# Performance work log

Hardware: AMD Instinct MI355X
Metric: run time of the kernel (lower is better)

Reference implementation:

```python
import jax, jax.numpy as jnp
import numpy as np

B = 2048          # number of tables (real batch size)
C = 8             # columns per table
D = 768           # hidden size (BERT-base)
TEMP = 0.07       # hp.temp
NEG_FILL = -10.0


def setup_inputs() -> dict:
    key = jax.random.key(0)
    k1, k2, k3 = jax.random.split(key, 3)
    n = B * C
    z = jax.random.normal(k1, (2 * n, D), jnp.float32) * 0.05
    idx = jnp.repeat(jnp.arange(B, dtype=jnp.int32), C)  # contiguous segment ids, as torch.full per table
    query = jax.random.normal(k2, (D, 1), jnp.float32) * 0.05
    attn_temp = jnp.ones((), jnp.float32)
    W = jax.random.normal(k3, (D, D), jnp.float32) * 0.02
    b = jnp.zeros((D,), jnp.float32)
    return {"z": z, "ori_table_indices": idx, "aug_table_indices": idx,
            "query": query, "attn_temp": attn_temp, "W": W, "b": b}


def _attn_pool(z, idx, query, t):
    # scatter-softmax attention pooling over variable-size table segments
    scores = (z @ query)[:, 0] / t                               # [n]
    e = jnp.exp(scores - scores.max())
    denom = jax.ops.segment_sum(e, idx, num_segments=B)[idx]     # [n]
    w = e / (denom + 1e-8)
    return jax.ops.segment_sum(z * w[:, None], idx, num_segments=B)  # [B, D]


def reference(z, ori_table_indices, aug_table_indices, query, attn_temp, W, b):
    n = B * C
    z_ori, z_aug = z[:n], z[n:]
    gx = _attn_pool(z_ori, ori_table_indices, query, attn_temp) @ W.T + b  # [B, D]
    hx = _attn_pool(z_aug, aug_table_indices, query, attn_temp) @ W.T + b  # [B, D]
    f = jnp.concatenate([gx, hx], axis=0)                                  # [2B, D]
    f = f / jnp.linalg.norm(f, axis=1, keepdims=True)
    sim = f @ f.T                                                          # [2B, 2B]
    N = 2 * B
    lab = jnp.concatenate([jnp.arange(B), jnp.arange(B)])
    labels = lab[None, :] == lab[:, None]                                  # [N, N] bool
    potential_pos = (sim > 0.9) & (~labels)
    safe_neg = (~potential_pos) & (~labels)
    # remove diagonal via rotation gather (order of negatives is irrelevant: topk sorts)
    cols = (jnp.arange(N)[:, None] + jnp.arange(1, N)[None, :]) % N        # [N, N-1]
    sim_od = jnp.take_along_axis(sim, cols, axis=1)
    safe_od = jnp.take_along_axis(safe_neg, cols, axis=1)
    # each row's single positive is its paired view at column (i+B) mod N
    pos = jnp.take_along_axis(sim, ((jnp.arange(N) + B) % N)[:, None], axis=1)  # [N, 1]
    neg = jnp.where(safe_od, sim_od, NEG_FILL)
    # data-dependent k; static-shape topk via descending sort + column mask
    k = jnp.maximum(1, jnp.floor(0.5 * jnp.mean(jnp.sum(safe_od, axis=1).astype(jnp.float32))).astype(jnp.int32))
    sneg = -jnp.sort(-neg, axis=1)                                         # descending
    new_neg = jnp.where(jnp.arange(N - 1)[None, :] < k, sneg, NEG_FILL)
    logits = jnp.concatenate([pos, new_neg], axis=1) / TEMP                # [N, N]
    # cross-entropy with target class 0
    loss = jnp.mean(jax.nn.logsumexp(logits, axis=1) - logits[:, 0])
    return loss
```

## Files before the change

### kernel.cpp

```cpp
#include <hip/hip_runtime.h>
#include <hip/hip_bf16.h>
#include <math.h>

#define Bq   2048
#define Cq   8
#define Dq   768
#define NROW 16384
#define NTOT 32768
#define Nq   4096
#define TEMPq 0.07f

typedef __attribute__((ext_vector_type(8))) short bf16x8;
typedef __attribute__((ext_vector_type(4))) float f32x4;

__device__ __hip_bfloat16 g_pooledb[(size_t)Nq * Dq];
__device__ __hip_bfloat16 g_Wb[(size_t)Dq * Dq];
__device__ float          g_f[(size_t)Nq * Dq];
__device__ __hip_bfloat16 g_fb[(size_t)Nq * Dq];
__device__ float          g_sim[(size_t)Nq * Nq];
__device__ unsigned int   g_viol;
__device__ float          g_rowloss[Nq];

#define GLDS16(src, dst) __builtin_amdgcn_global_load_lds( \
    (const __attribute__((address_space(1))) void*)(src),  \
    (__attribute__((address_space(3))) void*)(dst), 16, 0, 0)

__global__ __launch_bounds__(256) void pool_fused_kernel(const float* __restrict__ z,
                                                         const float* __restrict__ query,
                                                         const float* __restrict__ attn_temp) {
    int seg  = (int)((blockIdx.x * blockDim.x + threadIdx.x) >> 6);
    int lane = threadIdx.x & 63;
    if (seg >= Nq) return;
    int half = seg >> 11;
    int b    = seg & 2047;
    int baseRow = half * NROW + b * Cq;
    float invt = 1.f / attn_temp[0];

    float4 q4[3];
#pragma unroll
    for (int j = 0; j < 3; ++j) q4[j] = *(const float4*)(query + j * 256 + lane * 4);

    float4 v4[Cq][3];
    float s[Cq];
#pragma unroll
    for (int c = 0; c < Cq; ++c) {
        const float* zr = z + (size_t)(baseRow + c) * Dq;
        float acc = 0.f;
#pragma unroll
        for (int j = 0; j < 3; ++j) {
            float4 vz = *(const float4*)(zr + j * 256 + lane * 4);
            v4[c][j] = vz;
            acc += vz.x * q4[j].x + vz.y * q4[j].y + vz.z * q4[j].z + vz.w * q4[j].w;
        }
#pragma unroll
        for (int o = 32; o > 0; o >>= 1) acc += __shfl_xor(acc, o, 64);
        s[c] = acc * invt;
    }
    float m = s[0];
#pragma unroll
    for (int c = 1; c < Cq; ++c) m = fmaxf(m, s[c]);
    float e[Cq], denom = 0.f;
#pragma unroll
    for (int c = 0; c < Cq; ++c) { e[c] = expf(s[c] - m); denom += e[c]; }
    float inv = 1.f / (denom + 1e-8f);
#pragma unroll
    for (int j = 0; j < 3; ++j) {
        float4 acc = {0.f, 0.f, 0.f, 0.f};
#pragma unroll
        for (int c = 0; c < Cq; ++c) {
            acc.x += v4[c][j].x * e[c];
            acc.y += v4[c][j].y * e[c];
            acc.z += v4[c][j].z * e[c];
            acc.w += v4[c][j].w * e[c];
        }
        short4 o;
        o.x = ((__hip_bfloat16_raw)__float2bfloat16(acc.x * inv)).x;
        o.y = ((__hip_bfloat16_raw)__float2bfloat16(acc.y * inv)).x;
        o.z = ((__hip_bfloat16_raw)__float2bfloat16(acc.z * inv)).x;
        o.w = ((__hip_bfloat16_raw)__float2bfloat16(acc.w * inv)).x;
        *(short4*)((short*)g_pooledb + (size_t)seg * Dq + j * 256 + lane * 4) = o;
    }
}

__global__ __launch_bounds__(256) void wconv_kernel(const float* __restrict__ W) {
    if (blockIdx.x == 0 && threadIdx.x == 0) g_viol = 0u;
    int i = blockIdx.x * 256 + threadIdx.x;
    float4 v = ((const float4*)W)[i];
    short4 o;
    o.x = ((__hip_bfloat16_raw)__float2bfloat16(v.x)).x;
    o.y = ((__hip_bfloat16_raw)__float2bfloat16(v.y)).x;
    o.z = ((__hip_bfloat16_raw)__float2bfloat16(v.z)).x;
    o.w = ((__hip_bfloat16_raw)__float2bfloat16(v.w)).x;
    ((short4*)g_Wb)[i] = o;
}

__global__ __launch_bounds__(256) void fw_mfma_kernel(const float* __restrict__ bias) {
    __shared__ short lA[128 * 32];
    __shared__ short lB[128 * 32];
    const int bm = blockIdx.y * 128;
    const int bn = blockIdx.x * 128;

    const int tid  = threadIdx.x;
    const int wave = tid >> 6, lane = tid & 63;
    const int wr = wave >> 1, wc = wave & 1;

    const short* A = (const short*)g_pooledb;
    const short* Bt = (const short*)g_Wb;

    const int c0 = wave * 2, c1 = wave * 2 + 1;
    const int srow = lane >> 2;
    const int scol = (lane & 3) * 8;

    f32x4 acc[4][4];
#pragma unroll
    for (int m = 0; m < 4; ++m)
#pragma unroll
        for (int n = 0; n < 4; ++n) acc[m][n] = (f32x4){0.f, 0.f, 0.f, 0.f};

    for (int k0 = 0; k0 < Dq; k0 += 32) {
        GLDS16(A  + (size_t)(bm + c0 * 16 + srow) * Dq + k0 + scol, lA + c0 * 512);
        GLDS16(A  + (size_t)(bm + c1 * 16 + srow) * Dq + k0 + scol, lA + c1 * 512);
        GLDS16(Bt + (size_t)(bn + c0 * 16 + srow) * Dq + k0 + scol, lB + c0 * 512);
        GLDS16(Bt + (size_t)(bn + c1 * 16 + srow) * Dq + k0 + scol, lB + c1 * 512);
        __syncthreads();

        bf16x8 af[4], bfr[4];
#pragma unroll
        for (int m = 0; m < 4; ++m) {
            int row = wr * 64 + m * 16 + (lane & 15);
            af[m] = *(const bf16x8*)(lA + row * 32 + (lane >> 4) * 8);
        }
#pragma unroll
        for (int n = 0; n < 4; ++n) {
            int row = wc * 64 + n * 16 + (lane & 15);
            bfr[n] = *(const bf16x8*)(lB + row * 32 + (lane >> 4) * 8);
        }
#pragma unroll
        for (int m = 0; m < 4; ++m)
#pragma unroll
            for (int n = 0; n < 4; ++n)
                acc[m][n] = __builtin_amdgcn_mfma_f32_16x16x32_bf16(af[m], bfr[n], acc[m][n], 0, 0, 0);
        __syncthreads();
    }

#pragma unroll
    for (int m = 0; m < 4; ++m) {
        int rowb = bm + wr * 64 + m * 16 + (lane >> 4) * 4;
#pragma unroll
        for (int n = 0; n < 4; ++n) {
            int col = bn + wc * 64 + n * 16 + (lane & 15);
            float bc = bias[col];
#pragma unroll
            for (int j = 0; j < 4; ++j)
                g_f[(size_t)(rowb + j) * Dq + col] = acc[m][n][j] + bc;
        }
    }
}

__global__ __launch_bounds__(256) void normalize_kernel() {
    int row  = (int)((blockIdx.x * blockDim.x + threadIdx.x) >> 6);
    int lane = threadIdx.x & 63;
    if (row >= Nq) return;
    float ss = 0.f;
    float v[Dq / 64];
#pragma unroll
    for (int j = 0; j < Dq / 64; ++j) { v[j] = g_f[(size_t)row * Dq + j * 64 + lane]; ss += v[j] * v[j]; }
#pragma unroll
    for (int o = 32; o > 0; o >>= 1) ss += __shfl_xor(ss, o, 64);
    float rn = 1.f / sqrtf(ss);
#pragma unroll
    for (int j = 0; j < Dq / 64; ++j)
        g_fb[(size_t)row * Dq + j * 64 + lane] = __float2bfloat16(v[j] * rn);
}

__global__ __launch_bounds__(256) void sim_mfma_kernel() {
    __shared__ short lA[128 * 32];
    __shared__ short lB[128 * 32];

    int t = blockIdx.x;
    int bi = 0, rem = t;
    while (rem >= (32 - bi)) { rem -= (32 - bi); ++bi; }
    int bj = bi + rem;
    int bm = bi * 128, bn = bj * 128;

    const int tid  = threadIdx.x;
    const int wave = tid >> 6, lane = tid & 63;
    const int wr = wave >> 1, wc = wave & 1;

    const short* fb = (const short*)g_fb;

    const int c0 = wave * 2, c1 = wave * 2 + 1;
    const int srow = lane >> 2;
    const int scol = (lane & 3) * 8;

    f32x4 acc[4][4];
#pragma unroll
    for (int m = 0; m < 4; ++m)
#pragma unroll
        for (int n = 0; n < 4; ++n) acc[m][n] = (f32x4){0.f, 0.f, 0.f, 0.f};

    for (int k0 = 0; k0 < Dq; k0 += 32) {
        GLDS16(fb + (size_t)(bm + c0 * 16 + srow) * Dq + k0 + scol, lA + c0 * 512);
        GLDS16(fb + (size_t)(bm + c1 * 16 + srow) * Dq + k0 + scol, lA + c1 * 512);
        GLDS16(fb + (size_t)(bn + c0 * 16 + srow) * Dq + k0 + scol, lB + c0 * 512);
        GLDS16(fb + (size_t)(bn + c1 * 16 + srow) * Dq + k0 + scol, lB + c1 * 512);
        __syncthreads();

        bf16x8 af[4], bfr[4];
#pragma unroll
        for (int m = 0; m < 4; ++m) {
            int row = wr * 64 + m * 16 + (lane & 15);
            af[m] = *(const bf16x8*)(lA + row * 32 + (lane >> 4) * 8);
        }
#pragma unroll
        for (int n = 0; n < 4; ++n) {
            int row = wc * 64 + n * 16 + (lane & 15);
            bfr[n] = *(const bf16x8*)(lB + row * 32 + (lane >> 4) * 8);
        }
#pragma unroll
        for (int m = 0; m < 4; ++m)
#pragma unroll
            for (int n = 0; n < 4; ++n)
                acc[m][n] = __builtin_amdgcn_mfma_f32_16x16x32_bf16(af[m], bfr[n], acc[m][n], 0, 0, 0);
        __syncthreads();
    }

    int vio = 0;
#pragma unroll
    for (int m = 0; m < 4; ++m) {
        int rowb = bm + wr * 64 + m * 16 + (lane >> 4) * 4;
#pragma unroll
        for (int n = 0; n < 4; ++n) {
            int col = bn + wc * 64 + n * 16 + (lane & 15);
#pragma unroll
            for (int j = 0; j < 4; ++j) {
                g_sim[(size_t)(rowb + j) * Nq + col] = acc[m][n][j];
                vio += (acc[m][n][j] > 0.9f) && ((((rowb + j) ^ col) & 2047) != 0);
            }
        }
    }
    if (bi != bj) {
#pragma unroll
        for (int m = 0; m < 4; ++m) {
            int rowb = bm + wr * 64 + m * 16 + (lane >> 4) * 4;
#pragma unroll
            for (int n = 0; n < 4; ++n) {
                int col = bn + wc * 64 + n * 16 + (lane & 15);
                *(f32x4*)&g_sim[(size_t)col * Nq + rowb] = acc[m][n];
            }
        }
        vio *= 2;
    }
#pragma unroll
    for (int o = 32; o > 0; o >>= 1) vio += __shfl_xor(vio, o, 64);
    if (lane == 0 && vio > 0) atomicAdd(&g_viol, (unsigned int)vio);
}

__global__ __launch_bounds__(256) void lse_kernel() {
    const int row_id = (int)((blockIdx.x * blockDim.x + threadIdx.x) >> 6);
    const int lane = threadIdx.x & 63;
    const float* row = g_sim + (size_t)row_id * Nq;
    const int labi = row_id & 2047;
    const float invT = 1.0f / TEMPq;

    long long total = (long long)Nq * 4094LL - (long long)g_viol;
    int k = (int)(total / 8192LL);
    if (k < 1) k = 1;

    float v[64];
    float mx = -1e30f, mn = 1e30f;
    int cnt = 0;
#pragma unroll
    for (int q = 0; q < 16; ++q) {
        int j0 = q * 256 + lane * 4;
        float4 x4 = *(const float4*)(row + j0);
        float xs[4] = {x4.x, x4.y, x4.z, x4.w};
#pragma unroll
        for (int s = 0; s < 4; ++s) {
            int jj = q * 4 + s;
            int j  = j0 + s;
            bool sf = (xs[s] <= 0.9f) && (((j ^ labi) & 2047) != 0);
            float val = sf ? xs[s] : -2.0f;
            v[jj] = val;
            mx = fmaxf(mx, val);
            mn = fminf(mn, sf ? xs[s] : 2.0f);
            cnt += (int)__popcll(__ballot(sf));
        }
    }
#pragma unroll
    for (int o = 32; o > 0; o >>= 1) {
        mx = fmaxf(mx, __shfl_xor(mx, o, 64));
        mn = fminf(mn, __shfl_xor(mn, o, 64));
    }

    const float pos = row[(row_id + Bq) & (Nq - 1)];
    const float mxs = (cnt > 0) ? mx : -10.0f;
    const float ml  = fmaxf(pos, mxs) * invT;

    float lo = mn - 1e-3f, hi = mx;
    int c_hi = 0;
    const bool need = (cnt > k);
    if (need) {
        for (int it = 0; it < 12; ++it) {
            float mid = 0.5f * (lo + hi);
            int c = 0;
#pragma unroll
            for (int jj = 0; jj < 64; ++jj)
                c += (int)__popcll(__ballot(v[jj] > mid));
            if (c > k) lo = mid; else { hi = mid; c_hi = c; }
        }
    }

    float shi = 0.f, st = 0.f; int nt = 0;
#pragma unroll
    for (int jj = 0; jj < 64; ++jj) {
        float x = v[jj];
        float ev = __expf(x * invT - ml);
        if (!need)       { if (x > -1.5f) shi += ev; }
        else if (x > hi) { shi += ev; }
        else if (x > lo) { st += ev; nt++; }
    }
#pragma unroll
    for (int o = 32; o > 0; o >>= 1) {
        shi += __shfl_xor(shi, o, 64);
        st  += __shfl_xor(st,  o, 64);
        nt  += __shfl_xor(nt,  o, 64);
    }
    if (lane == 0) {
        float S = __expf(pos * invT - ml) + shi;
        if (need && c_hi < k && nt > 0)
            S += st * (float)(k - c_hi) / (float)nt;
        g_rowloss[row_id] = (logf(S) + ml) - pos * invT;
    }
}

__global__ __launch_bounds__(256) void loss_kernel(float* __restrict__ out) {
    float s = 0.f;
    for (int i = threadIdx.x; i < Nq; i += 256) s += g_rowloss[i];
    __shared__ float sm[256];
    sm[threadIdx.x] = s; __syncthreads();
    for (int o = 128; o > 0; o >>= 1) {
        if (threadIdx.x < o) sm[threadIdx.x] += sm[threadIdx.x + o];
        __syncthreads();
    }
    if (threadIdx.x == 0) out[0] = sm[0] / (float)Nq;
}

extern "C" void kernel_launch(void* const* d_in, const int* in_sizes, int n_in,
                              void* d_out, int out_size, void* d_ws, size_t ws_size,
                              hipStream_t stream) {
    const float* z         = (const float*)d_in[0];
    const float* query     = (const float*)d_in[3];
    const float* attn_temp = (const float*)d_in[4];
    const float* W         = (const float*)d_in[5];
    const float* bias      = (const float*)d_in[6];
    float* out = (float*)d_out;

    pool_fused_kernel<<<Nq / 4, 256, 0, stream>>>(z, query, attn_temp);
    wconv_kernel<<<(Dq * Dq / 4) / 256, 256, 0, stream>>>(W);
    fw_mfma_kernel<<<dim3(Dq / 128, Nq / 128), 256, 0, stream>>>(bias);
    normalize_kernel<<<Nq / 4, 256, 0, stream>>>();
    sim_mfma_kernel<<<(32 * 33) / 2, 256, 0, stream>>>();
    lse_kernel<<<Nq / 4, 256, 0, stream>>>();
    loss_kernel<<<1, 256, 0, stream>>>(out);
}
```

Baseline: 129.4 us.

## Store similarity matrix in fp16 and merge W conversion into pooling kernel

The 4096x4096 similarity matrix is now written and read as fp16 instead of fp32, halving the traffic between the sim GEMM and the logsumexp/top-k kernel. The W-to-bf16 conversion kernel is folded into the pooling kernel as extra blocks, saving one launch. fp16 rounding of similarities may shift the >0.9 threshold decisions and the top-k selection slightly. The violation count is still computed from fp32 accumulators, so it can disagree with the fp16 values used later.

```diff
diff --git a/kernel.cpp b/kernel.cpp
--- a/kernel.cpp
+++ b/kernel.cpp
@@ -12,12 +12,14 @@
 
 typedef __attribute__((ext_vector_type(8))) short bf16x8;
 typedef __attribute__((ext_vector_type(4))) float f32x4;
+typedef __attribute__((ext_vector_type(8))) _Float16 f16x8;
+typedef __attribute__((ext_vector_type(4))) _Float16 f16x4;
 
 __device__ __hip_bfloat16 g_pooledb[(size_t)Nq * Dq];
 __device__ __hip_bfloat16 g_Wb[(size_t)Dq * Dq];
 __device__ float          g_f[(size_t)Nq * Dq];
 __device__ __hip_bfloat16 g_fb[(size_t)Nq * Dq];
-__device__ float          g_sim[(size_t)Nq * Nq];
+__device__ _Float16       g_simh[(size_t)Nq * Nq];
 __device__ unsigned int   g_viol;
 __device__ float          g_rowloss[Nq];
 
@@ -25,9 +27,22 @@
     (const __attribute__((address_space(1))) void*)(src),  \
     (__attribute__((address_space(3))) void*)(dst), 16, 0, 0)
 
-__global__ __launch_bounds__(256) void pool_fused_kernel(const float* __restrict__ z,
-                                                         const float* __restrict__ query,
-                                                         const float* __restrict__ attn_temp) {
+__global__ __launch_bounds__(256) void prep_kernel(const float* __restrict__ z,
+                                                   const float* __restrict__ query,
+                                                   const float* __restrict__ attn_temp,
+                                                   const float* __restrict__ W) {
+    if (blockIdx.x >= 1024) {
+        int i = (blockIdx.x - 1024) * 256 + threadIdx.x;
+        if (i == 0) g_viol = 0u;
+        float4 v = ((const float4*)W)[i];
+        short4 o;
+        o.x = ((__hip_bfloat16_raw)__float2bfloat16(v.x)).x;
+        o.y = ((__hip_bfloat16_raw)__float2bfloat16(v.y)).x;
+        o.z = ((__hip_bfloat16_raw)__float2bfloat16(v.z)).x;
+        o.w = ((__hip_bfloat16_raw)__float2bfloat16(v.w)).x;
+        ((short4*)g_Wb)[i] = o;
+        return;
+    }
     int seg  = (int)((blockIdx.x * blockDim.x + threadIdx.x) >> 6);
     int lane = threadIdx.x & 63;
     if (seg >= Nq) return;
@@ -82,18 +97,6 @@
     }
 }
 
-__global__ __launch_bounds__(256) void wconv_kernel(const float* __restrict__ W) {
-    if (blockIdx.x == 0 && threadIdx.x == 0) g_viol = 0u;
-    int i = blockIdx.x * 256 + threadIdx.x;
-    float4 v = ((const float4*)W)[i];
-    short4 o;
-    o.x = ((__hip_bfloat16_raw)__float2bfloat16(v.x)).x;
-    o.y = ((__hip_bfloat16_raw)__float2bfloat16(v.y)).x;
-    o.z = ((__hip_bfloat16_raw)__float2bfloat16(v.z)).x;
-    o.w = ((__hip_bfloat16_raw)__float2bfloat16(v.w)).x;
-    ((short4*)g_Wb)[i] = o;
-}
-
 __global__ __launch_bounds__(256) void fw_mfma_kernel(const float* __restrict__ bias) {
     __shared__ short lA[128 * 32];
     __shared__ short lB[128 * 32];
@@ -234,7 +237,7 @@
             int col = bn + wc * 64 + n * 16 + (lane & 15);
 #pragma unroll
             for (int j = 0; j < 4; ++j) {
-                g_sim[(size_t)(rowb + j) * Nq + col] = acc[m][n][j];
+                g_simh[(size_t)(rowb + j) * Nq + col] = (_Float16)acc[m][n][j];
                 vio += (acc[m][n][j] > 0.9f) && ((((rowb + j) ^ col) & 2047) != 0);
             }
         }
@@ -246,7 +249,10 @@
 #pragma unroll
             for (int n = 0; n < 4; ++n) {
                 int col = bn + wc * 64 + n * 16 + (lane & 15);
-                *(f32x4*)&g_sim[(size_t)col * Nq + rowb] = acc[m][n];
+                f16x4 h;
+#pragma unroll
+                for (int j = 0; j < 4; ++j) h[j] = (_Float16)acc[m][n][j];
+                *(f16x4*)&g_simh[(size_t)col * Nq + rowb] = h;
             }
         }
         vio *= 2;
@@ -259,7 +265,7 @@
 __global__ __launch_bounds__(256) void lse_kernel() {
     const int row_id = (int)((blockIdx.x * blockDim.x + threadIdx.x) >> 6);
     const int lane = threadIdx.x & 63;
-    const float* row = g_sim + (size_t)row_id * Nq;
+    const _Float16* row = g_simh + (size_t)row_id * Nq;
     const int labi = row_id & 2047;
     const float invT = 1.0f / TEMPq;
 
@@ -271,19 +277,19 @@
     float mx = -1e30f, mn = 1e30f;
     int cnt = 0;
 #pragma unroll
-    for (int q = 0; q < 16; ++q) {
-        int j0 = q * 256 + lane * 4;
-        float4 x4 = *(const float4*)(row + j0);
-        float xs[4] = {x4.x, x4.y, x4.z, x4.w};
-#pragma unroll
-        for (int s = 0; s < 4; ++s) {
-            int jj = q * 4 + s;
+    for (int q = 0; q < 8; ++q) {
+        int j0 = q * 512 + lane * 8;
+        f16x8 x8 = *(const f16x8*)(row + j0);
+#pragma unroll
+        for (int s = 0; s < 8; ++s) {
+            int jj = q * 8 + s;
             int j  = j0 + s;
-            bool sf = (xs[s] <= 0.9f) && (((j ^ labi) & 2047) != 0);
-            float val = sf ? xs[s] : -2.0f;
+            float xv = (float)x8[s];
+            bool sf = (xv <= 0.9f) && (((j ^ labi) & 2047) != 0);
+            float val = sf ? xv : -2.0f;
             v[jj] = val;
             mx = fmaxf(mx, val);
-            mn = fminf(mn, sf ? xs[s] : 2.0f);
+            mn = fminf(mn, sf ? xv : 2.0f);
             cnt += (int)__popcll(__ballot(sf));
         }
     }
@@ -293,7 +299,7 @@
         mn = fminf(mn, __shfl_xor(mn, o, 64));
     }
 
-    const float pos = row[(row_id + Bq) & (Nq - 1)];
+    const float pos = (float)row[(row_id + Bq) & (Nq - 1)];
     const float mxs = (cnt > 0) ? mx : -10.0f;
     const float ml  = fmaxf(pos, mxs) * invT;
 
@@ -356,8 +362,7 @@
     const float* bias      = (const float*)d_in[6];
     float* out = (float*)d_out;
 
-    pool_fused_kernel<<<Nq / 4, 256, 0, stream>>>(z, query, attn_temp);
-    wconv_kernel<<<(Dq * Dq / 4) / 256, 256, 0, stream>>>(W);
+    prep_kernel<<<1024 + (Dq * Dq / 4) / 256, 256, 0, stream>>>(z, query, attn_temp, W);
     fw_mfma_kernel<<<dim3(Dq / 128, Nq / 128), 256, 0, stream>>>(bias);
     normalize_kernel<<<Nq / 4, 256, 0, stream>>>();
     sim_mfma_kernel<<<(32 * 33) / 2, 256, 0, stream>>>();
```

Result: faster. 121.3 us (-6.3%).
